# Kernel optimization log

Hardware: AMD Instinct MI355X
Metric: run time of the kernel (lower is better)

Reference implementation:

```python
import jax, jax.numpy as jnp
import numpy as np


def setup_inputs() -> dict:
    key = jax.random.key(0)
    kx, kw, kb = jax.random.split(key, 3)
    B, D, L, W = 2, 4096, 4096, 4
    # int8 quantized input / weight / bias (stored as int8, full [-128,127] range)
    x = jax.random.randint(kx, (B, D, L), -128, 128, dtype=jnp.int32).astype(jnp.int8)
    weight = jax.random.randint(kw, (D, W), -128, 128, dtype=jnp.int32).astype(jnp.int8)
    bias = jax.random.randint(kb, (D,), -128, 128, dtype=jnp.int32).astype(jnp.int8)
    return {
        "x": x,
        "weight": weight,
        "bias": bias,
        "input_scale": jnp.float32(0.05),
        "weight_scale": jnp.float32(0.002),
        "output_scale": jnp.float32(0.05),
        "bias_scale": jnp.float32(0.01),
    }


def _causal_dw_conv(xf, wf):
    # xf: [B, D, L] float, wf: [D, W] float; depthwise causal conv (left pad W-1)
    D, W = wf.shape
    return jax.lax.conv_general_dilated(
        xf, wf[:, None, :],  # [D, 1, W] OIH with feature_group_count=D -> depthwise
        window_strides=(1,), padding=[(W - 1, 0)],
        dimension_numbers=("NCH", "OIH", "NCH"), feature_group_count=D)


def reference(x, weight, bias, input_scale, weight_scale, output_scale, bias_scale):
    # fused dequant -> causal depthwise conv -> bias -> SiLU -> requant to int8
    xf = x.astype(jnp.float32) * input_scale
    wf = weight.astype(jnp.float32) * weight_scale
    bf = bias.astype(jnp.float32) * bias_scale
    y = _causal_dw_conv(xf, wf) + bf[None, :, None]
    y = jax.nn.silu(y)  # causal_conv1d activation=True -> SiLU
    q = jnp.clip(jnp.round(y / output_scale), -128.0, 127.0).astype(jnp.int8)
    return q
```

## Files before the change

### kernel.cpp

```cpp
#include <hip/hip_runtime.h>


#define LMASK 4095
#define DMASK 4095
#define LSHIFT 12

typedef int iv4 __attribute__((ext_vector_type(4)));

__device__ __forceinline__ int silu_requant(float y, float inv_out) {
    float e = __expf(-y);
    float s = y * __builtin_amdgcn_rcpf(1.0f + e);
    float q = rintf(s * inv_out);
    q = fminf(fmaxf(q, -128.0f), 127.0f);
    return (int)q;
}

__global__ __launch_bounds__(256) void qconv1d_kernel(
    const int* __restrict__ x,
    const int* __restrict__ w,
    const int* __restrict__ bias,
    const float* __restrict__ in_s_p,
    const float* __restrict__ w_s_p,
    const float* __restrict__ out_s_p,
    const float* __restrict__ b_s_p,
    int* __restrict__ out)
{
    const int t    = blockIdx.x * blockDim.x + threadIdx.x;
    const int base = t << 2;
    const int e    = t << 4;
    const int pos  = e & LMASK;
    const int d    = (e >> LSHIFT) & DMASK;

    const iv4* __restrict__ xv = (const iv4*)x;

    iv4 c0 = xv[base + 0];
    iv4 c1 = xv[base + 1];
    iv4 c2 = xv[base + 2];
    iv4 c3 = xv[base + 3];
    iv4 h  = (iv4){0, 0, 0, 0};
    if (pos != 0) h = xv[base - 1];

    const int dw = __builtin_amdgcn_readfirstlane(d);
    iv4 wv = ((const iv4*)w)[dw];
    const float bias_i = (float)bias[dw];

    const float w0 = (float)wv.x, w1 = (float)wv.y, w2 = (float)wv.z, w3 = (float)wv.w;

    float s[19];
    s[0] = (float)h.y;  s[1] = (float)h.z;  s[2] = (float)h.w;
    s[3]  = (float)c0.x; s[4]  = (float)c0.y; s[5]  = (float)c0.z; s[6]  = (float)c0.w;
    s[7]  = (float)c1.x; s[8]  = (float)c1.y; s[9]  = (float)c1.z; s[10] = (float)c1.w;
    s[11] = (float)c2.x; s[12] = (float)c2.y; s[13] = (float)c2.z; s[14] = (float)c2.w;
    s[15] = (float)c3.x; s[16] = (float)c3.y; s[17] = (float)c3.z; s[18] = (float)c3.w;

    const float in_s  = in_s_p[0];
    const float w_s   = w_s_p[0];
    const float out_s = out_s_p[0];
    const float b_s   = b_s_p[0];

    const float s_xw    = in_s * w_s;
    const float inv_out = 1.0f / out_s;
    const float bf      = bias_i * b_s;

    int q[16];
#pragma unroll
    for (int i = 0; i < 16; ++i) {
        float a = w0 * s[i] + w1 * s[i + 1] + w2 * s[i + 2] + w3 * s[i + 3];
        q[i] = silu_requant(a * s_xw + bf, inv_out);
    }

    iv4* ov = (iv4*)out;
    ov[base + 0] = (iv4){q[0],  q[1],  q[2],  q[3]};
    ov[base + 1] = (iv4){q[4],  q[5],  q[6],  q[7]};
    ov[base + 2] = (iv4){q[8],  q[9],  q[10], q[11]};
    ov[base + 3] = (iv4){q[12], q[13], q[14], q[15]};
}

extern "C" void kernel_launch(void* const* d_in, const int* in_sizes, int n_in,
                              void* d_out, int out_size, void* d_ws, size_t ws_size,
                              hipStream_t stream) {
    const int*   x    = (const int*)d_in[0];
    const int*   w    = (const int*)d_in[1];
    const int*   bias = (const int*)d_in[2];
    const float* is   = (const float*)d_in[3];
    const float* ws   = (const float*)d_in[4];
    const float* os   = (const float*)d_in[5];
    const float* bs   = (const float*)d_in[6];
    int* out = (int*)d_out;

    const int threads = out_size >> 4;
    const int block   = 256;
    const int grid    = threads / block;

    qconv1d_kernel<<<grid, block, 0, stream>>>(x, w, bias, is, ws, os, bs, out);
}
```

Before: 245.8 us.

## Map one block per row with coalesced strided vector loads and stores

Each block now handles one (batch, channel) row of 4096 elements, and each thread processes four int4 vectors spaced 256 apart instead of 16 contiguous elements. Adjacent lanes therefore touch adjacent 16-byte vectors, so global loads and stores coalesce fully. The causal halo comes from re-reading the previous vector, which is mostly a cache hit but doubles load instructions. Weight and bias indexing now uses blockIdx directly, so readfirstlane is no longer needed.

```diff
diff --git a/kernel.cpp b/kernel.cpp
--- a/kernel.cpp
+++ b/kernel.cpp
@@ -1,9 +1,7 @@
 #include <hip/hip_runtime.h>
 
 
-#define LMASK 4095
 #define DMASK 4095
-#define LSHIFT 12
 
 typedef int iv4 __attribute__((ext_vector_type(4)));
 
@@ -25,33 +23,30 @@
     const float* __restrict__ b_s_p,
     int* __restrict__ out)
 {
-    const int t    = blockIdx.x * blockDim.x + threadIdx.x;
-    const int base = t << 2;
-    const int e    = t << 4;
-    const int pos  = e & LMASK;
-    const int d    = (e >> LSHIFT) & DMASK;
+    const int tid  = threadIdx.x;
+    const int row  = blockIdx.x;
+    const int d    = row & DMASK;
+    const int rcb  = row << 10;
 
     const iv4* __restrict__ xv = (const iv4*)x;
 
-    iv4 c0 = xv[base + 0];
-    iv4 c1 = xv[base + 1];
-    iv4 c2 = xv[base + 2];
-    iv4 c3 = xv[base + 3];
-    iv4 h  = (iv4){0, 0, 0, 0};
-    if (pos != 0) h = xv[base - 1];
+    iv4 cur[4], prv[4];
+#pragma unroll
+    for (int j = 0; j < 4; ++j)
+        cur[j] = xv[rcb + (j << 8) + tid];
 
-    const int dw = __builtin_amdgcn_readfirstlane(d);
-    iv4 wv = ((const iv4*)w)[dw];
-    const float bias_i = (float)bias[dw];
+    {
+        iv4 p = (iv4){0, 0, 0, 0};
+        if (tid != 0) p = xv[rcb + tid - 1];
+        prv[0] = p;
+    }
+#pragma unroll
+    for (int j = 1; j < 4; ++j)
+        prv[j] = xv[rcb + (j << 8) + tid - 1];
 
+    iv4 wv = ((const iv4*)w)[d];
     const float w0 = (float)wv.x, w1 = (float)wv.y, w2 = (float)wv.z, w3 = (float)wv.w;
-
-    float s[19];
-    s[0] = (float)h.y;  s[1] = (float)h.z;  s[2] = (float)h.w;
-    s[3]  = (float)c0.x; s[4]  = (float)c0.y; s[5]  = (float)c0.z; s[6]  = (float)c0.w;
-    s[7]  = (float)c1.x; s[8]  = (float)c1.y; s[9]  = (float)c1.z; s[10] = (float)c1.w;
-    s[11] = (float)c2.x; s[12] = (float)c2.y; s[13] = (float)c2.z; s[14] = (float)c2.w;
-    s[15] = (float)c3.x; s[16] = (float)c3.y; s[17] = (float)c3.z; s[18] = (float)c3.w;
+    const float bias_i = (float)bias[d];
 
     const float in_s  = in_s_p[0];
     const float w_s   = w_s_p[0];
@@ -62,18 +57,27 @@
     const float inv_out = 1.0f / out_s;
     const float bf      = bias_i * b_s;
 
-    int q[16];
+    iv4* __restrict__ ov = (iv4*)out;
+
 #pragma unroll
-    for (int i = 0; i < 16; ++i) {
-        float a = w0 * s[i] + w1 * s[i + 1] + w2 * s[i + 2] + w3 * s[i + 3];
-        q[i] = silu_requant(a * s_xw + bf, inv_out);
+    for (int j = 0; j < 4; ++j) {
+        float sm3 = (float)prv[j].y, sm2 = (float)prv[j].z, sm1 = (float)prv[j].w;
+        float s0 = (float)cur[j].x, s1 = (float)cur[j].y,
+              s2 = (float)cur[j].z, s3 = (float)cur[j].w;
+
+        float a0 = w0*sm3 + w1*sm2 + w2*sm1 + w3*s0;
+        float a1 = w0*sm2 + w1*sm1 + w2*s0  + w3*s1;
+        float a2 = w0*sm1 + w1*s0  + w2*s1  + w3*s2;
+        float a3 = w0*s0  + w1*s1  + w2*s2  + w3*s3;
+
+        iv4 q;
+        q.x = silu_requant(a0 * s_xw + bf, inv_out);
+        q.y = silu_requant(a1 * s_xw + bf, inv_out);
+        q.z = silu_requant(a2 * s_xw + bf, inv_out);
+        q.w = silu_requant(a3 * s_xw + bf, inv_out);
+
+        ov[rcb + (j << 8) + tid] = q;
     }
-
-    iv4* ov = (iv4*)out;
-    ov[base + 0] = (iv4){q[0],  q[1],  q[2],  q[3]};
-    ov[base + 1] = (iv4){q[4],  q[5],  q[6],  q[7]};
-    ov[base + 2] = (iv4){q[8],  q[9],  q[10], q[11]};
-    ov[base + 3] = (iv4){q[12], q[13], q[14], q[15]};
 }
 
 extern "C" void kernel_launch(void* const* d_in, const int* in_sizes, int n_in,
@@ -88,9 +92,8 @@
     const float* bs   = (const float*)d_in[6];
     int* out = (int*)d_out;
 
-    const int threads = out_size >> 4;
-    const int block   = 256;
-    const int grid    = threads / block;
+    const int rows  = out_size >> 12;
+    const int block = 256;
 
-    qconv1d_kernel<<<grid, block, 0, stream>>>(x, w, bias, is, ws, os, bs, out);
+    qconv1d_kernel<<<rows, block, 0, stream>>>(x, w, bias, is, ws, os, bs, out);
 }
```

After: 236.9 us. 3.6% less time.
